# Kernel tuning notes

Hardware: AMD Instinct MI355X
Metric: run time of the kernel (lower is better)

The kernel has to match this reference:

```python
import jax, jax.numpy as jnp
import numpy as np

# hyp2f1 parameters of the Mann eddy-lifetime model: 2F1(1/3, 17/6, 4/3, -(kL)^-2)
A_P = 1.0 / 3.0
B_P = 17.0 / 6.0
C_P = 4.0 / 3.0
N_TERMS = 1000  # series terms; tail ~ N^{-2.5} -> ~1e-8 rel. error


def _hyp2f1_pfaff_series(w):
    """2F1(1/3, -3/2, 4/3, w) for w in [0, 1] via its power series.

    This is the Pfaff-transformed series; terms decay like n^{-3.5} * w^n,
    so a fixed N_TERMS truncation is accurate over the whole range.
    """
    a, bp, c = A_P, C_P - B_P, C_P  # bp = -3/2

    def body(carry, n):
        s, term = carry
        term = term * ((a + n) * (bp + n)) / ((c + n) * (n + 1.0)) * w
        return (s + term, term), None

    init = (jnp.ones_like(w), jnp.ones_like(w))
    (s, _), _ = jax.lax.scan(body, init, jnp.arange(N_TERMS, dtype=w.dtype))
    return s


def _mann_hyp2f1(t):
    """2F1(1/3, 17/6, 4/3, -t^-2) for t > 0 via the Pfaff transformation.

    2F1(a,b,c,z) = (1-z)^{-a} 2F1(a, c-b, c, z/(z-1)) with z = -1/t^2,
    so z/(z-1) = 1/(1+t^2) in (0,1) and (1-z) = (1+t^2)/t^2.
    """
    t2 = t * t
    w = 1.0 / (1.0 + t2)
    pref = (t2 * w) ** A_P  # (1-z)^{-a}
    return pref * _hyp2f1_pfaff_series(w)


def setup_inputs() -> dict:
    key = jax.random.key(0)
    k = jax.random.normal(key, (256, 256, 128, 3), dtype=jnp.float32)
    L = jnp.ones((), dtype=jnp.float32)
    gamma = jnp.ones((), dtype=jnp.float32)
    return {"k": k, "L": L, "gamma": gamma}


def reference(k, L, gamma):
    # Original detaches k and L (tau is non-differentiable); only gamma carries grad.
    k_s = jax.lax.stop_gradient(k)
    L_s = jax.lax.stop_gradient(L)
    k_norm = jnp.linalg.norm(k_s, axis=-1)  # [256,256,128]
    kL = L_s * k_norm
    mask = kL > 0.0
    safe_t = jnp.where(mask, kL, 1.0)
    F = _mann_hyp2f1(safe_t)
    tau = jnp.where(mask, safe_t ** (-2.0 / 3.0) / jnp.sqrt(F), 0.0)
    return gamma * tau
```

## Files before the change

### kernel.cpp

```cpp
#include <hip/hip_runtime.h>
#include <math.h>


typedef float f4 __attribute__((ext_vector_type(4)));

constexpr int NT = 48;

struct CoefArr { float v[NT]; };

constexpr CoefArr gen_coefs() {
    CoefArr r{};
    double term = 1.0;
    r.v[0] = 1.0f;
    for (int n = 0; n + 1 < NT; ++n) {
        const double a  = 1.0 / 3.0;
        const double bp = -1.5;
        const double c  = 4.0 / 3.0;
        term *= ((a + n) * (bp + n)) / ((c + n) * (n + 1.0));
        r.v[n + 1] = (float)term;
    }
    return r;
}

constexpr CoefArr COEF = gen_coefs();

__device__ __forceinline__ float mann_tau(float t2) {
    float w = __builtin_amdgcn_rcpf(1.0f + t2);
    float s = COEF.v[NT - 1];
#pragma unroll
    for (int n = NT - 2; n >= 0; --n) s = fmaf(s, w, COEF.v[n]);
    float cw = __builtin_amdgcn_exp2f(__builtin_amdgcn_logf(w) * (1.0f / 3.0f));
    return __builtin_amdgcn_rsqf(t2 * cw * s);
}

__global__ __launch_bounds__(256) void mann_elt_kernel(
    const float* __restrict__ k,
    const float* __restrict__ Lp,
    const float* __restrict__ gp,
    float* __restrict__ out,
    int n)
{
    const int  t        = threadIdx.x;
    const long blockPts = (long)blockIdx.x * 1024;

    const float L  = Lp[0];
    const float g  = gp[0];
    const float L2 = L * L;

    __shared__ f4 sk4[768];

    if (blockPts + 1024 <= (long)n) {
        const f4* kg    = (const f4*)k;
        const long base4 = blockPts * 3 / 4;
#pragma unroll
        for (int i = 0; i < 3; ++i)
            sk4[t + i * 256] = kg[base4 + t + i * 256];
        __syncthreads();

        const float* skf = (const float*)sk4;
        const f4*    sp  = (const f4*)(skf + t * 12);
        f4 p0 = sp[0];
        f4 p1 = sp[1];
        f4 p2 = sp[2];

        float n2[4];
        n2[0] = fmaf(p0[0], p0[0], fmaf(p0[1], p0[1], p0[2] * p0[2]));
        n2[1] = fmaf(p0[3], p0[3], fmaf(p1[0], p1[0], p1[1] * p1[1]));
        n2[2] = fmaf(p1[2], p1[2], fmaf(p1[3], p1[3], p2[0] * p2[0]));
        n2[3] = fmaf(p2[1], p2[1], fmaf(p2[2], p2[2], p2[3] * p2[3]));

        f4 o;
#pragma unroll
        for (int j = 0; j < 4; ++j) {
            float t2  = L2 * n2[j];
            float tau = mann_tau(t2);
            o[j] = (t2 > 0.0f) ? g * tau : 0.0f;
        }
        __builtin_nontemporal_store(o, (f4*)(out + blockPts) + t);
    } else {
        for (int j = 0; j < 4; ++j) {
            const long i = blockPts + (long)t * 4 + j;
            if (i >= (long)n) break;
            float kx = k[3 * i + 0];
            float ky = k[3 * i + 1];
            float kz = k[3 * i + 2];
            float t2  = L2 * (kx * kx + ky * ky + kz * kz);
            float tau = mann_tau(t2);
            out[i] = (t2 > 0.0f) ? g * tau : 0.0f;
        }
    }
}

extern "C" void kernel_launch(void* const* d_in, const int* in_sizes, int n_in,
                              void* d_out, int out_size, void* d_ws, size_t ws_size,
                              hipStream_t stream) {
    const float* k  = (const float*)d_in[0];
    const float* L  = (const float*)d_in[1];
    const float* g  = (const float*)d_in[2];
    float* out = (float*)d_out;

    const int n = out_size;
    const int block = 256;
    const int ptsPerBlock = 1024;
    const int grid = (n + ptsPerBlock - 1) / ptsPerBlock;

    mann_elt_kernel<<<grid, block, 0, stream>>>(k, L, g, out, n);
}
```

Before: 155.2 us.

## Persistent grid with double-buffered async global-to-LDS tile prefetch

Replaces the one-tile-per-block launch with a persistent grid of at most 2048 blocks that loop over 1024-point tiles. Each next tile is prefetched straight into a second LDS buffer with global_load_lds while the current tile is computed, so memory latency can overlap the Horner evaluation. Points are now read from LDS at stride 3 and written with scalar coalesced nontemporal stores. The leftover partial tile is handled by block 0 alone. The cost is more loop and synchronisation overhead per block, and correctness depends on the barrier also waiting for the async LDS loads.

```diff
diff --git a/kernel.cpp b/kernel.cpp
--- a/kernel.cpp
+++ b/kernel.cpp
@@ -4,7 +4,12 @@
 
 typedef float f4 __attribute__((ext_vector_type(4)));
 
-constexpr int NT = 48;
+typedef const __attribute__((address_space(1))) void* gas_ptr;
+typedef __attribute__((address_space(3))) void* las_ptr;
+
+constexpr int NT       = 48;
+constexpr int TILE_PTS = 1024;
+constexpr int TILE_F4  = 768;
 
 struct CoefArr { float v[NT]; };
 
@@ -33,6 +38,16 @@
     return __builtin_amdgcn_rsqf(t2 * cw * s);
 }
 
+__device__ __forceinline__ void stage_tile(f4* ldsDst, const f4* gSrc, int tid) {
+#pragma unroll
+    for (int i = 0; i < 3; ++i) {
+        __builtin_amdgcn_global_load_lds(
+            (gas_ptr)(gSrc + i * 256 + tid),
+            (las_ptr)(ldsDst + i * 256 + tid),
+            16, 0, 0);
+    }
+}
+
 __global__ __launch_bounds__(256) void mann_elt_kernel(
     const float* __restrict__ k,
     const float* __restrict__ Lp,
@@ -40,47 +55,59 @@
     float* __restrict__ out,
     int n)
 {
-    const int  t        = threadIdx.x;
-    const long blockPts = (long)blockIdx.x * 1024;
+    const int tid    = threadIdx.x;
+    const int ntiles = n / TILE_PTS;
+
+    __shared__ f4 buf[2][TILE_F4];
 
     const float L  = Lp[0];
     const float g  = gp[0];
     const float L2 = L * L;
 
-    __shared__ f4 sk4[768];
+    const f4* kg = (const f4*)k;
 
-    if (blockPts + 1024 <= (long)n) {
-        const f4* kg    = (const f4*)k;
-        const long base4 = blockPts * 3 / 4;
-#pragma unroll
-        for (int i = 0; i < 3; ++i)
-            sk4[t + i * 256] = kg[base4 + t + i * 256];
+    int tile = blockIdx.x;
+    const int stride = gridDim.x;
+
+    if (tile < ntiles)
+        stage_tile(buf[0], kg + (size_t)tile * TILE_F4, tid);
+
+    int cur = 0;
+    for (; tile < ntiles; tile += stride) {
         __syncthreads();
+        const int nxt = tile + stride;
+        if (nxt < ntiles)
+            stage_tile(buf[cur ^ 1], kg + (size_t)nxt * TILE_F4, tid);
 
-        const float* skf = (const float*)sk4;
-        const f4*    sp  = (const f4*)(skf + t * 12);
-        f4 p0 = sp[0];
-        f4 p1 = sp[1];
-        f4 p2 = sp[2];
+        const float* s = (const float*)buf[cur];
+        const long outBase = (long)tile * TILE_PTS + tid;
 
-        float n2[4];
-        n2[0] = fmaf(p0[0], p0[0], fmaf(p0[1], p0[1], p0[2] * p0[2]));
-        n2[1] = fmaf(p0[3], p0[3], fmaf(p1[0], p1[0], p1[1] * p1[1]));
-        n2[2] = fmaf(p1[2], p1[2], fmaf(p1[3], p1[3], p2[0] * p2[0]));
-        n2[3] = fmaf(p2[1], p2[1], fmaf(p2[2], p2[2], p2[3] * p2[3]));
-
-        f4 o;
+        float x[4], y[4], z[4];
 #pragma unroll
         for (int j = 0; j < 4; ++j) {
-            float t2  = L2 * n2[j];
+            const int p = tid + j * 256;
+            x[j] = s[3 * p + 0];
+            y[j] = s[3 * p + 1];
+            z[j] = s[3 * p + 2];
+        }
+
+        float r[4];
+#pragma unroll
+        for (int j = 0; j < 4; ++j) {
+            float t2  = L2 * fmaf(x[j], x[j], fmaf(y[j], y[j], z[j] * z[j]));
             float tau = mann_tau(t2);
-            o[j] = (t2 > 0.0f) ? g * tau : 0.0f;
+            r[j] = (t2 > 0.0f) ? g * tau : 0.0f;
         }
-        __builtin_nontemporal_store(o, (f4*)(out + blockPts) + t);
-    } else {
-        for (int j = 0; j < 4; ++j) {
-            const long i = blockPts + (long)t * 4 + j;
-            if (i >= (long)n) break;
+
+#pragma unroll
+        for (int j = 0; j < 4; ++j)
+            __builtin_nontemporal_store(r[j], out + outBase + j * 256);
+
+        cur ^= 1;
+    }
+
+    if (blockIdx.x == 0) {
+        for (long i = (long)ntiles * TILE_PTS + tid; i < (long)n; i += 256) {
             float kx = k[3 * i + 0];
             float ky = k[3 * i + 1];
             float kz = k[3 * i + 2];
@@ -99,10 +126,9 @@
     const float* g  = (const float*)d_in[2];
     float* out = (float*)d_out;
 
-    const int n = out_size;
-    const int block = 256;
-    const int ptsPerBlock = 1024;
-    const int grid = (n + ptsPerBlock - 1) / ptsPerBlock;
+    const int n      = out_size;
+    const int ntiles = n / TILE_PTS;
+    int grid = ntiles < 2048 ? (ntiles > 0 ? ntiles : 1) : 2048;
 
-    mann_elt_kernel<<<grid, block, 0, stream>>>(k, L, g, out, n);
+    mann_elt_kernel<<<grid, 256, 0, stream>>>(k, L, g, out, n);
 }
```

After: 159.3 us. +2.6%, slower.
